# Performance work log

Measured on AMD Instinct MI355X. Metric: run time of the kernel, lower is better.

Reference implementation:

```python
import jax, jax.numpy as jnp
import numpy as np

B, P, C = 64, 196, 768   # batch, num_patches, hidden_size
HS = 384                 # hidden_s (token-mixing hidden dim)
NG = 8                   # num_grids
GMIN, GMAX = -1.0, 1.0


def _rbf(x):
    # fast-KAN radial basis: exp(-((x - grid_i)/denom)^2), grid over [GMIN, GMAX]
    grid = jnp.linspace(GMIN, GMAX, NG).astype(x.dtype)
    denom = (GMAX - GMIN) / (NG - 1)
    return jnp.exp(-jnp.square((x[..., None] - grid) / denom))  # [..., din, NG]


def _kan_linear(x, spline_w, base_w, base_b):
    # x: [..., din]; spline_w: [dout, din*NG]; base_w: [dout, din]; base_b: [dout]
    basis = _rbf(x).reshape(*x.shape[:-1], -1)          # [..., din*NG]
    out = basis @ spline_w.T                            # spline term (no bias)
    out = out + jax.nn.silu(x) @ base_w.T + base_b      # base update term
    return out


def setup_inputs() -> dict:
    key = jax.random.key(0)
    ks = jax.random.split(key, 5)
    s = 0.1  # spline_weight_init_scale
    return {
        "x": jax.random.normal(ks[0], (B, P, C), jnp.float32),
        "fc1_spline_w": jax.random.normal(ks[1], (HS, P * NG), jnp.float32) * (s / np.sqrt(P * NG)),
        "fc1_base_w": jax.random.normal(ks[2], (HS, P), jnp.float32) / np.sqrt(P),
        "fc1_base_b": jnp.zeros((HS,), jnp.float32),
        "fc2_spline_w": jax.random.normal(ks[3], (P, HS * NG), jnp.float32) * (s / np.sqrt(HS * NG)),
        "fc2_base_w": jax.random.normal(ks[4], (P, HS), jnp.float32) / np.sqrt(HS),
        "fc2_base_b": jnp.zeros((P,), jnp.float32),
    }


def reference(x, fc1_spline_w, fc1_base_w, fc1_base_b,
              fc2_spline_w, fc2_base_w, fc2_base_b):
    skip_param = 1.0
    # token mixing: permute so KANLinear acts over the patch axis
    h = jnp.swapaxes(x, 1, 2)                                   # [B, C, P]
    h = _kan_linear(h, fc1_spline_w, fc1_base_w, fc1_base_b)    # [B, C, HS]
    # dropout p=0 -> identity; the two intermediate permutes cancel
    h = _kan_linear(h, fc2_spline_w, fc2_base_w, fc2_base_b)    # [B, C, P]
    out = jnp.swapaxes(h, 1, 2)                                 # [B, P, C]
    return out + skip_param * x
```

## Files before the change

### kernel.cpp

```cpp
#include <hip/hip_runtime.h>
#include <cstdint>

#define B_  64
#define P_  196
#define C_  768
#define HS_ 384
#define M_  49152

#define NC1 13
#define KT1 111
#define NT1 12
#define NC2 24
#define KT2 216
#define NT2 7

#define H1_ELEMS  ((size_t)M_ * HS_)
#define W1P_ELEMS ((size_t)KT1 * NT1 * 512)
#define W2P_ELEMS ((size_t)KT2 * NT2 * 512)

typedef __attribute__((ext_vector_type(8)))  short short8;
typedef __attribute__((ext_vector_type(16))) float f32x16;

#define MFMA(w, a, c) __builtin_amdgcn_mfma_f32_32x32x16_bf16((w), (a), (c), 0, 0, 0)

static __device__ __forceinline__ float bf2f(unsigned short u) {
    union { unsigned int i; float f; } v; v.i = ((unsigned int)u) << 16; return v.f;
}
static __device__ __forceinline__ unsigned short f2bf_rne(float f) {
    union { float f; unsigned int i; } v; v.f = f;
    unsigned int r = v.i + 0x7FFFu + ((v.i >> 16) & 1u);
    return (unsigned short)(r >> 16);
}
static __device__ __forceinline__ unsigned int pack2(float a, float b) {
    unsigned int ua = __float_as_uint(a) + 0x8000u;
    unsigned int ub = __float_as_uint(b) + 0x8000u;
    return __builtin_amdgcn_perm(ub, ua, 0x07060302u);
}
static __device__ __forceinline__ short8 rbf8(float s) {
    float t0 = 3.5f * s + 3.5f;
    union { short8 s8; unsigned int u[4]; } r;
#pragma unroll
    for (int q = 0; q < 4; q++) {
        float d0 = t0 - (float)(2 * q);
        float d1 = t0 - (float)(2 * q + 1);
        r.u[q] = pack2(__expf(-d0 * d0), __expf(-d1 * d1));
    }
    return r.s8;
}
static __device__ __forceinline__ unsigned int silu2(float a, float b) {
    float fa = a * __builtin_amdgcn_rcpf(1.f + __expf(-a));
    float fb = b * __builtin_amdgcn_rcpf(1.f + __expf(-b));
    return pack2(fa, fb);
}

__global__ void pack_w_kernel(const float* __restrict__ w1s,
                              const float* __restrict__ w1b,
                              const float* __restrict__ w2s,
                              const float* __restrict__ w2b,
                              unsigned short* __restrict__ w1p,
                              unsigned short* __restrict__ w2p) {
    size_t idx = (size_t)blockIdx.x * 256 + threadIdx.x;
    if (idx < W1P_ELEMS) {
        int j    = idx & 7;
        int lane = (idx >> 3) & 63;
        int lin  = idx >> 9;
        int nt   = lin % NT1;
        int tt   = lin / NT1;
        int cc   = (tt < 108) ? tt / 9 : 12;
        int kk   = (tt < 108) ? tt % 9 : (tt - 108);
        int ktl  = (cc < 12) ? kk : ((kk < 2) ? kk : 8);
        int n = nt * 32 + (lane & 31);
        int khalf = lane >> 5;
        float v = 0.f;
        if (ktl < 8) {
            int p = cc * 16 + ktl * 2 + khalf;
            if (p < P_) v = w1s[(size_t)n * 1568 + p * 8 + j];
        } else {
            int p = cc * 16 + khalf * 8 + j;
            if (p < P_) v = w1b[(size_t)n * 196 + p];
        }
        w1p[idx] = f2bf_rne(v);
    } else {
        size_t idx2 = idx - W1P_ELEMS;
        if (idx2 < W2P_ELEMS) {
            int j    = idx2 & 7;
            int lane = (idx2 >> 3) & 63;
            int lin  = idx2 >> 9;
            int nt   = lin % NT2;
            int tt   = lin / NT2;
            int cc   = tt / 9;
            int ktl  = tt % 9;
            int n = nt * 32 + (lane & 31);
            int khalf = lane >> 5;
            float v = 0.f;
            if (n < P_) {
                if (ktl < 8) {
                    int s = cc * 16 + ktl * 2 + khalf;
                    v = w2s[(size_t)n * 3072 + s * 8 + j];
                } else {
                    int s = cc * 16 + khalf * 8 + j;
                    v = w2b[(size_t)n * 384 + s];
                }
            }
            w2p[idx2] = f2bf_rne(v);
        }
    }
}

#define FB_  9216

__global__ __launch_bounds__(256, 2)
void fc1_kernel(const float* __restrict__ x,
                const unsigned short* __restrict__ w1p,
                const float* __restrict__ b1,
                unsigned short* __restrict__ h1t) {
    __shared__ __align__(16) unsigned short frag[2 * FB_];
    int blk = blockIdx.x;
    int tid = threadIdx.x;
    int b   = blk / 12;
    int c0  = (blk % 12) * 64;
    const float* xb = x + (size_t)b * (P_ * C_);

    int pr  = tid & 63;
    int sg  = tid >> 6;
    int prt = pr >> 5, pl31 = pr & 31;
    int pbase_rbf  = (prt << 9) + pl31 * 8;
    int pbase_silu = 8 * 1024 + (prt << 9) + (((sg >> 1) << 5) | pl31) * 8 + (sg & 1) * 4;

    int wave = sg, lane = tid & 63;
    int l31 = lane & 31, half = lane >> 5;
    int nt0 = wave * 3;

    f32x16 acc[2][3];
#pragma unroll
    for (int rt = 0; rt < 2; rt++)
#pragma unroll
        for (int nt = 0; nt < 3; nt++)
#pragma unroll
            for (int i = 0; i < 16; i++) acc[rt][nt][i] = 0.f;

    const short8* wp = (const short8*)w1p;
    short8 wbuf[3][3];

    auto wload = [&](int d, const short8* wt0, int kk) {
        const short8* wt = wt0 + (size_t)kk * (NT1 * 64);
        wbuf[d][0] = wt[0]; wbuf[d][1] = wt[64]; wbuf[d][2] = wt[128];
    };
    auto produce = [&](int fb, const float (&rb)[4]) {
#pragma unroll
        for (int i = 0; i < 4; i++) {
            int sl = sg * 4 + i;
            *(short8*)&frag[fb + (sl >> 1) * 1024 + ((sl & 1) << 8) + pbase_rbf] = rbf8(rb[i]);
        }
        uint2 sv;
        sv.x = silu2(rb[0], rb[1]);
        sv.y = silu2(rb[2], rb[3]);
        *(uint2*)&frag[fb + pbase_silu] = sv;
    };
    auto do_mfma = [&](short8 w0, short8 w1, short8 w2, short8 a0, short8 a1) {
        acc[0][0] = MFMA(w0, a0, acc[0][0]); acc[1][0] = MFMA(w0, a1, acc[1][0]);
        acc[0][1] = MFMA(w1, a0, acc[0][1]); acc[1][1] = MFMA(w1, a1, acc[1][1]);
        acc[0][2] = MFMA(w2, a0, acc[0][2]); acc[1][2] = MFMA(w2, a1, acc[1][2]);
    };
    auto consume = [&](int fb, const short8* wt0) {
        const unsigned short* fg = &frag[fb];
        short8 a0 = *(const short8*)&fg[lane * 8];
        short8 a1 = *(const short8*)&fg[512 + lane * 8];
#pragma unroll
        for (int kk = 0; kk < 9; kk++) {
            short8 na0, na1;
            if (kk < 8) {
                na0 = *(const short8*)&fg[(kk + 1) * 1024 + lane * 8];
                na1 = *(const short8*)&fg[(kk + 1) * 1024 + 512 + lane * 8];
            }
            short8 w0 = wbuf[kk % 3][0], w1 = wbuf[kk % 3][1], w2 = wbuf[kk % 3][2];
            if (kk < 6) wload(kk % 3, wt0, kk + 3);
            do_mfma(w0, w1, w2, a0, a1);
            if (kk < 8) { a0 = na0; a1 = na1; }
        }
    };
    auto body = [&](int cc, const float (&rbP)[4], float (&rbL)[4]) {
#pragma unroll
        for (int i = 0; i < 4; i++) {
            int p = (cc + 2) * 16 + sg * 4 + i;
            p = (p < P_) ? p : (P_ - 1);
            rbL[i] = xb[(size_t)p * C_ + c0 + pr];
        }
        const short8* wt0 = wp + ((size_t)(cc * 9) * NT1 + nt0) * 64 + lane;
        wload(0, wt0, 0); wload(1, wt0, 1); wload(2, wt0, 2);
        produce(((cc + 1) & 1) * FB_, rbP);
        consume((cc & 1) * FB_, wt0);
        __syncthreads();
    };

    float rbA[4], rbB[4];
#pragma unroll
    for (int i = 0; i < 4; i++) {
        rbA[i] = xb[(size_t)(sg * 4 + i) * C_ + c0 + pr];
        rbB[i] = xb[(size_t)(16 + sg * 4 + i) * C_ + c0 + pr];
    }
    produce(0, rbA);
    __syncthreads();

    for (int c2 = 0; c2 < 6; c2++) {
        body(2 * c2,     rbB, rbA);
        body(2 * c2 + 1, rbA, rbB);
    }
    {
        const short8* wt0 = wp + ((size_t)108 * NT1 + nt0) * 64 + lane;
        wload(0, wt0, 0); wload(1, wt0, 1); wload(2, wt0, 2);
        const unsigned short* fg = &frag[0];
#pragma unroll
        for (int kk = 0; kk < 3; kk++) {
            int ktl = (kk < 2) ? kk : 8;
            short8 a0 = *(const short8*)&fg[ktl * 1024 + lane * 8];
            short8 a1 = *(const short8*)&fg[ktl * 1024 + 512 + lane * 8];
            do_mfma(wbuf[kk][0], wbuf[kk][1], wbuf[kk][2], a0, a1);
        }
    }

#pragma unroll
    for (int nt = 0; nt < 3; nt++) {
        int n0 = (nt0 + nt) * 32 + 4 * half;
#pragma unroll
        for (int reg = 0; reg < 16; reg++) {
            int n = n0 + (reg & 3) + 8 * (reg >> 2);
            float bv = b1[n];
#pragma unroll
            for (int rt = 0; rt < 2; rt++) {
                h1t[(size_t)n * M_ + blk * 64 + rt * 32 + l31] = f2bf_rne(acc[rt][nt][reg] + bv);
            }
        }
    }
}

__global__ __launch_bounds__(256, 2)
void fc2_kernel(const unsigned short* __restrict__ h1t,
                const unsigned short* __restrict__ w2p,
                const float* __restrict__ b2,
                const float* __restrict__ x,
                float* __restrict__ out) {
    __shared__ __align__(16) unsigned short frag[2 * FB_];
    int blk = blockIdx.x;
    int tid = threadIdx.x;
    int rbase = blk * 64;

    int pr  = tid & 63;
    int sg  = tid >> 6;
    int prt = pr >> 5, pl31 = pr & 31;
    int pbase_rbf  = (prt << 9) + pl31 * 8;
    int pbase_silu = 8 * 1024 + (prt << 9) + (((sg >> 1) << 5) | pl31) * 8 + (sg & 1) * 4;

    int wave = sg, lane = tid & 63;
    int l31 = lane & 31, half = lane >> 5;
    int nt0 = wave * 2;
    int ntn = (wave < 3) ? 2 : 1;
    int off1 = (ntn > 1) ? 64 : 0;

    f32x16 acc[2][2];
#pragma unroll
    for (int rt = 0; rt < 2; rt++)
#pragma unroll
        for (int nt = 0; nt < 2; nt++)
#pragma unroll
            for (int i = 0; i < 16; i++) acc[rt][nt][i] = 0.f;

    const short8* wp = (const short8*)w2p;
    short8 wbuf[3][2];

    auto wload = [&](int d, const short8* wt0, int kk) {
        const short8* wt = wt0 + (size_t)kk * (NT2 * 64);
        wbuf[d][0] = wt[0]; wbuf[d][1] = wt[off1];
    };
    auto produce = [&](int fb, const unsigned short (&rb)[4]) {
        float v0 = bf2f(rb[0]), v1 = bf2f(rb[1]), v2 = bf2f(rb[2]), v3 = bf2f(rb[3]);
        float vv[4] = {v0, v1, v2, v3};
#pragma unroll
        for (int i = 0; i < 4; i++) {
            int sl = sg * 4 + i;
            *(short8*)&frag[fb + (sl >> 1) * 1024 + ((sl & 1) << 8) + pbase_rbf] = rbf8(vv[i]);
        }
        uint2 sv;
        sv.x = silu2(v0, v1);
        sv.y = silu2(v2, v3);
        *(uint2*)&frag[fb + pbase_silu] = sv;
    };
    auto do_mfma = [&](short8 w0, short8 w1, short8 a0, short8 a1) {
        acc[0][0] = MFMA(w0, a0, acc[0][0]); acc[1][0] = MFMA(w0, a1, acc[1][0]);
        acc[0][1] = MFMA(w1, a0, acc[0][1]); acc[1][1] = MFMA(w1, a1, acc[1][1]);
    };
    auto consume = [&](int fb, const short8* wt0) {
        const unsigned short* fg = &frag[fb];
        short8 a0 = *(const short8*)&fg[lane * 8];
        short8 a1 = *(const short8*)&fg[512 + lane * 8];
#pragma unroll
        for (int kk = 0; kk < 9; kk++) {
            short8 na0, na1;
            if (kk < 8) {
                na0 = *(const short8*)&fg[(kk + 1) * 1024 + lane * 8];
                na1 = *(const short8*)&fg[(kk + 1) * 1024 + 512 + lane * 8];
            }
            short8 w0 = wbuf[kk % 3][0], w1 = wbuf[kk % 3][1];
            if (kk < 6) wload(kk % 3, wt0, kk + 3);
            do_mfma(w0, w1, a0, a1);
            if (kk < 8) { a0 = na0; a1 = na1; }
        }
    };
    auto body = [&](int cc, const unsigned short (&rbP)[4], unsigned short (&rbL)[4]) {
#pragma unroll
        for (int i = 0; i < 4; i++) {
            int s = (cc + 2) * 16 + sg * 4 + i;
            s = (s < HS_) ? s : (HS_ - 1);
            rbL[i] = h1t[(size_t)s * M_ + rbase + pr];
        }
        const short8* wt0 = wp + ((size_t)(cc * 9) * NT2 + nt0) * 64 + lane;
        wload(0, wt0, 0); wload(1, wt0, 1); wload(2, wt0, 2);
        if (cc + 1 < NC2) produce(((cc + 1) & 1) * FB_, rbP);
        consume((cc & 1) * FB_, wt0);
        __syncthreads();
    };

    unsigned short rbA[4], rbB[4];
#pragma unroll
    for (int i = 0; i < 4; i++) {
        rbA[i] = h1t[(size_t)(sg * 4 + i) * M_ + rbase + pr];
        rbB[i] = h1t[(size_t)(16 + sg * 4 + i) * M_ + rbase + pr];
    }
    produce(0, rbA);
    __syncthreads();

    for (int c2 = 0; c2 < 12; c2++) {
        body(2 * c2,     rbB, rbA);
        body(2 * c2 + 1, rbA, rbB);
    }

    int b = blk / 12;
    int c0 = (blk % 12) * 64;
#pragma unroll
    for (int nt = 0; nt < 2; nt++) {
        if (nt < ntn) {
            int p0 = (nt0 + nt) * 32 + 4 * half;
#pragma unroll
            for (int reg = 0; reg < 16; reg++) {
                int p = p0 + (reg & 3) + 8 * (reg >> 2);
                if (p < P_) {
                    float bv = b2[p];
#pragma unroll
                    for (int rt = 0; rt < 2; rt++) {
                        size_t off = ((size_t)b * P_ + p) * C_ + c0 + rt * 32 + l31;
                        out[off] = acc[rt][nt][reg] + bv + x[off];
                    }
                }
            }
        }
    }
}

extern "C" void kernel_launch(void* const* d_in, const int* in_sizes, int n_in,
                              void* d_out, int out_size, void* d_ws, size_t ws_size,
                              hipStream_t stream) {
    const float* x   = (const float*)d_in[0];
    const float* w1s = (const float*)d_in[1];
    const float* w1b = (const float*)d_in[2];
    const float* b1  = (const float*)d_in[3];
    const float* w2s = (const float*)d_in[4];
    const float* w2b = (const float*)d_in[5];
    const float* b2  = (const float*)d_in[6];
    float* out = (float*)d_out;

    unsigned short* h1t = (unsigned short*)d_ws;
    unsigned short* w1p = h1t + H1_ELEMS;
    unsigned short* w2p = w1p + W1P_ELEMS;

    int pack_blocks = (int)((W1P_ELEMS + W2P_ELEMS) / 256);
    pack_w_kernel<<<pack_blocks, 256, 0, stream>>>(w1s, w1b, w2s, w2b, w1p, w2p);
    fc1_kernel<<<M_ / 64, 256, 0, stream>>>(x, w1p, b1, h1t);
    fc2_kernel<<<M_ / 64, 256, 0, stream>>>(h1t, w2p, b2, x, out);
}
```

Baseline: 300.7 us.

## Double waves per block, splitting row tiles across waves in fc1 and fc2

```diff
diff --git a/kernel.cpp b/kernel.cpp
--- a/kernel.cpp
+++ b/kernel.cpp
@@ -109,7 +109,8 @@
 
 #define FB_  9216
 
-__global__ __launch_bounds__(256, 2)
+
+__global__ __launch_bounds__(512, 4)
 void fc1_kernel(const float* __restrict__ x,
                 const unsigned short* __restrict__ w1p,
                 const float* __restrict__ b1,
@@ -125,19 +126,19 @@
     int sg  = tid >> 6;
     int prt = pr >> 5, pl31 = pr & 31;
     int pbase_rbf  = (prt << 9) + pl31 * 8;
-    int pbase_silu = 8 * 1024 + (prt << 9) + (((sg >> 1) << 5) | pl31) * 8 + (sg & 1) * 4;
-
-    int wave = sg, lane = tid & 63;
+    int pbase_silu = 8 * 1024 + (prt << 9) + (((sg >> 2) << 5) | pl31) * 8 + (sg & 3) * 2;
+
+    int lane = tid & 63;
     int l31 = lane & 31, half = lane >> 5;
-    int nt0 = wave * 3;
-
-    f32x16 acc[2][3];
-#pragma unroll
-    for (int rt = 0; rt < 2; rt++)
-#pragma unroll
-        for (int nt = 0; nt < 3; nt++)
-#pragma unroll
-            for (int i = 0; i < 16; i++) acc[rt][nt][i] = 0.f;
+    int rt  = sg >> 2;
+    int nt0 = (sg & 3) * 3;
+    int abase = rt * 512 + lane * 8;
+
+    f32x16 acc[3];
+#pragma unroll
+    for (int nt = 0; nt < 3; nt++)
+#pragma unroll
+        for (int i = 0; i < 16; i++) acc[nt][i] = 0.f;
 
     const short8* wp = (const short8*)w1p;
     short8 wbuf[3][3];
@@ -146,43 +147,36 @@
         const short8* wt = wt0 + (size_t)kk * (NT1 * 64);
         wbuf[d][0] = wt[0]; wbuf[d][1] = wt[64]; wbuf[d][2] = wt[128];
     };
-    auto produce = [&](int fb, const float (&rb)[4]) {
-#pragma unroll
-        for (int i = 0; i < 4; i++) {
-            int sl = sg * 4 + i;
+    auto produce = [&](int fb, const float (&rb)[2]) {
+#pragma unroll
+        for (int i = 0; i < 2; i++) {
+            int sl = sg * 2 + i;
             *(short8*)&frag[fb + (sl >> 1) * 1024 + ((sl & 1) << 8) + pbase_rbf] = rbf8(rb[i]);
         }
-        uint2 sv;
-        sv.x = silu2(rb[0], rb[1]);
-        sv.y = silu2(rb[2], rb[3]);
-        *(uint2*)&frag[fb + pbase_silu] = sv;
-    };
-    auto do_mfma = [&](short8 w0, short8 w1, short8 w2, short8 a0, short8 a1) {
-        acc[0][0] = MFMA(w0, a0, acc[0][0]); acc[1][0] = MFMA(w0, a1, acc[1][0]);
-        acc[0][1] = MFMA(w1, a0, acc[0][1]); acc[1][1] = MFMA(w1, a1, acc[1][1]);
-        acc[0][2] = MFMA(w2, a0, acc[0][2]); acc[1][2] = MFMA(w2, a1, acc[1][2]);
+        *(unsigned int*)&frag[fb + pbase_silu] = silu2(rb[0], rb[1]);
+    };
+    auto do_mfma = [&](short8 w0, short8 w1, short8 w2, short8 a0) {
+        acc[0] = MFMA(w0, a0, acc[0]);
+        acc[1] = MFMA(w1, a0, acc[1]);
+        acc[2] = MFMA(w2, a0, acc[2]);
     };
     auto consume = [&](int fb, const short8* wt0) {
         const unsigned short* fg = &frag[fb];
-        short8 a0 = *(const short8*)&fg[lane * 8];
-        short8 a1 = *(const short8*)&fg[512 + lane * 8];
+        short8 a0 = *(const short8*)&fg[abase];
 #pragma unroll
         for (int kk = 0; kk < 9; kk++) {
-            short8 na0, na1;
-            if (kk < 8) {
-                na0 = *(const short8*)&fg[(kk + 1) * 1024 + lane * 8];
-                na1 = *(const short8*)&fg[(kk + 1) * 1024 + 512 + lane * 8];
-            }
+            short8 na0;
+            if (kk < 8) na0 = *(const short8*)&fg[(kk + 1) * 1024 + abase];
             short8 w0 = wbuf[kk % 3][0], w1 = wbuf[kk % 3][1], w2 = wbuf[kk % 3][2];
             if (kk < 6) wload(kk % 3, wt0, kk + 3);
-            do_mfma(w0, w1, w2, a0, a1);
-            if (kk < 8) { a0 = na0; a1 = na1; }
-        }
-    };
-    auto body = [&](int cc, const float (&rbP)[4], float (&rbL)[4]) {
-#pragma unroll
-        for (int i = 0; i < 4; i++) {
-            int p = (cc + 2) * 16 + sg * 4 + i;
+            do_mfma(w0, w1, w2, a0);
+            if (kk < 8) a0 = na0;
+        }
+    };
+    auto body = [&](int cc, const float (&rbP)[2], float (&rbL)[2]) {
+#pragma unroll
+        for (int i = 0; i < 2; i++) {
+            int p = (cc + 2) * 16 + sg * 2 + i;
             p = (p < P_) ? p : (P_ - 1);
             rbL[i] = xb[(size_t)p * C_ + c0 + pr];
         }
@@ -193,11 +187,11 @@
         __syncthreads();
     };
 
-    float rbA[4], rbB[4];
-#pragma unroll
-    for (int i = 0; i < 4; i++) {
-        rbA[i] = xb[(size_t)(sg * 4 + i) * C_ + c0 + pr];
-        rbB[i] = xb[(size_t)(16 + sg * 4 + i) * C_ + c0 + pr];
+    float rbA[2], rbB[2];
+#pragma unroll
+    for (int i = 0; i < 2; i++) {
+        rbA[i] = xb[(size_t)(sg * 2 + i) * C_ + c0 + pr];
+        rbB[i] = xb[(size_t)(16 + sg * 2 + i) * C_ + c0 + pr];
     }
     produce(0, rbA);
     __syncthreads();
@@ -213,9 +207,8 @@
 #pragma unroll
         for (int kk = 0; kk < 3; kk++) {
             int ktl = (kk < 2) ? kk : 8;
-            short8 a0 = *(const short8*)&fg[ktl * 1024 + lane * 8];
-            short8 a1 = *(const short8*)&fg[ktl * 1024 + 512 + lane * 8];
-            do_mfma(wbuf[kk][0], wbuf[kk][1], wbuf[kk][2], a0, a1);
+            short8 a0 = *(const short8*)&fg[ktl * 1024 + abase];
+            do_mfma(wbuf[kk][0], wbuf[kk][1], wbuf[kk][2], a0);
         }
     }
 
@@ -226,15 +219,12 @@
         for (int reg = 0; reg < 16; reg++) {
             int n = n0 + (reg & 3) + 8 * (reg >> 2);
             float bv = b1[n];
-#pragma unroll
-            for (int rt = 0; rt < 2; rt++) {
-                h1t[(size_t)n * M_ + blk * 64 + rt * 32 + l31] = f2bf_rne(acc[rt][nt][reg] + bv);
-            }
-        }
-    }
-}
-
-__global__ __launch_bounds__(256, 2)
+            h1t[(size_t)n * M_ + blk * 64 + rt * 32 + l31] = f2bf_rne(acc[nt][reg] + bv);
+        }
+    }
+}
+
+__global__ __launch_bounds__(512, 4)
 void fc2_kernel(const unsigned short* __restrict__ h1t,
                 const unsigned short* __restrict__ w2p,
                 const float* __restrict__ b2,
@@ -249,21 +239,22 @@
     int sg  = tid >> 6;
     int prt = pr >> 5, pl31 = pr & 31;
     int pbase_rbf  = (prt << 9) + pl31 * 8;
-    int pbase_silu = 8 * 1024 + (prt << 9) + (((sg >> 1) << 5) | pl31) * 8 + (sg & 1) * 4;
-
-    int wave = sg, lane = tid & 63;
+    int pbase_silu = 8 * 1024 + (prt << 9) + (((sg >> 2) << 5) | pl31) * 8 + (sg & 3) * 2;
+
+    int lane = tid & 63;
     int l31 = lane & 31, half = lane >> 5;
-    int nt0 = wave * 2;
-    int ntn = (wave < 3) ? 2 : 1;
-    int off1 = (ntn > 1) ? 64 : 0;
-
-    f32x16 acc[2][2];
-#pragma unroll
-    for (int rt = 0; rt < 2; rt++)
-#pragma unroll
-        for (int nt = 0; nt < 2; nt++)
-#pragma unroll
-            for (int i = 0; i < 16; i++) acc[rt][nt][i] = 0.f;
+    int rt  = sg >> 2;
+    int ntg = sg & 3;
+    int nt0 = ntg * 2;
+    bool two = (ntg < 3);
+    int off1 = two ? 64 : 0;
+    int abase = rt * 512 + lane * 8;
+
+    f32x16 acc[2];
+#pragma unroll
+    for (int nt = 0; nt < 2; nt++)
+#pragma unroll
+        for (int i = 0; i < 16; i++) acc[nt][i] = 0.f;
 
     const short8* wp = (const short8*)w2p;
     short8 wbuf[3][2];
@@ -272,44 +263,37 @@
         const short8* wt = wt0 + (size_t)kk * (NT2 * 64);
         wbuf[d][0] = wt[0]; wbuf[d][1] = wt[off1];
     };
-    auto produce = [&](int fb, const unsigned short (&rb)[4]) {
-        float v0 = bf2f(rb[0]), v1 = bf2f(rb[1]), v2 = bf2f(rb[2]), v3 = bf2f(rb[3]);
-        float vv[4] = {v0, v1, v2, v3};
-#pragma unroll
-        for (int i = 0; i < 4; i++) {
-            int sl = sg * 4 + i;
+    auto produce = [&](int fb, const unsigned short (&rb)[2]) {
+        float v0 = bf2f(rb[0]), v1 = bf2f(rb[1]);
+        float vv[2] = {v0, v1};
+#pragma unroll
+        for (int i = 0; i < 2; i++) {
+            int sl = sg * 2 + i;
             *(short8*)&frag[fb + (sl >> 1) * 1024 + ((sl & 1) << 8) + pbase_rbf] = rbf8(vv[i]);
         }
-        uint2 sv;
-        sv.x = silu2(v0, v1);
-        sv.y = silu2(v2, v3);
-        *(uint2*)&frag[fb + pbase_silu] = sv;
-    };
-    auto do_mfma = [&](short8 w0, short8 w1, short8 a0, short8 a1) {
-        acc[0][0] = MFMA(w0, a0, acc[0][0]); acc[1][0] = MFMA(w0, a1, acc[1][0]);
-        acc[0][1] = MFMA(w1, a0, acc[0][1]); acc[1][1] = MFMA(w1, a1, acc[1][1]);
+        *(unsigned int*)&frag[fb + pbase_silu] = silu2(v0, v1);
+    };
+    auto do_mfma = [&](short8 w0, short8 w1, short8 a0) {
+        acc[0] = MFMA(w0, a0, acc[0]);
+        if (two) acc[1] = MFMA(w1, a0, acc[1]);
     };
     auto consume = [&](int fb, const short8* wt0) {
         const unsigned short* fg = &frag[fb];
-        short8 a0 = *(const short8*)&fg[lane * 8];
-        short8 a1 = *(const short8*)&fg[512 + lane * 8];
+        short8 a0 = *(const short8*)&fg[abase];
 #pragma unroll
         for (int kk = 0; kk < 9; kk++) {
-            short8 na0, na1;
-            if (kk < 8) {
-                na0 = *(const short8*)&fg[(kk + 1) * 1024 + lane * 8];
-                na1 = *(const short8*)&fg[(kk + 1) * 1024 + 512 + lane * 8];
-            }
+            short8 na0;
+            if (kk < 8) na0 = *(const short8*)&fg[(kk + 1) * 1024 + abase];
             short8 w0 = wbuf[kk % 3][0], w1 = wbuf[kk % 3][1];
             if (kk < 6) wload(kk % 3, wt0, kk + 3);
-            do_mfma(w0, w1, a0, a1);
-            if (kk < 8) { a0 = na0; a1 = na1; }
-        }
-    };
-    auto body = [&](int cc, const unsigned short (&rbP)[4], unsigned short (&rbL)[4]) {
-#pragma unroll
-        for (int i = 0; i < 4; i++) {
-            int s = (cc + 2) * 16 + sg * 4 + i;
+            do_mfma(w0, w1, a0);
+            if (kk < 8) a0 = na0;
+        }
+    };
+    auto body = [&](int cc, const unsigned short (&rbP)[2], unsigned short (&rbL)[2]) {
+#pragma unroll
+        for (int i = 0; i < 2; i++) {
+            int s = (cc + 2) * 16 + sg * 2 + i;
             s = (s < HS_) ? s : (HS_ - 1);
             rbL[i] = h1t[(size_t)s * M_ + rbase + pr];
         }
@@ -320,11 +304,11 @@
         __syncthreads();
     };
 
-    unsigned short rbA[4], rbB[4];
-#pragma unroll
-    for (int i = 0; i < 4; i++) {
-        rbA[i] = h1t[(size_t)(sg * 4 + i) * M_ + rbase + pr];
-        rbB[i] = h1t[(size_t)(16 + sg * 4 + i) * M_ + rbase + pr];
+    unsigned short rbA[2], rbB[2];
+#pragma unroll
+    for (int i = 0; i < 2; i++) {
+        rbA[i] = h1t[(size_t)(sg * 2 + i) * M_ + rbase + pr];
+        rbB[i] = h1t[(size_t)(16 + sg * 2 + i) * M_ + rbase + pr];
     }
     produce(0, rbA);
     __syncthreads();
@@ -338,18 +322,15 @@
     int c0 = (blk % 12) * 64;
 #pragma unroll
     for (int nt = 0; nt < 2; nt++) {
-        if (nt < ntn) {
+        if (nt == 0 || two) {
             int p0 = (nt0 + nt) * 32 + 4 * half;
 #pragma unroll
             for (int reg = 0; reg < 16; reg++) {
                 int p = p0 + (reg & 3) + 8 * (reg >> 2);
                 if (p < P_) {
                     float bv = b2[p];
-#pragma unroll
-                    for (int rt = 0; rt < 2; rt++) {
-                        size_t off = ((size_t)b * P_ + p) * C_ + c0 + rt * 32 + l31;
-                        out[off] = acc[rt][nt][reg] + bv + x[off];
-                    }
+                    size_t off = ((size_t)b * P_ + p) * C_ + c0 + rt * 32 + l31;
+                    out[off] = acc[nt][reg] + bv + x[off];
                 }
             }
         }
@@ -374,6 +355,6 @@
 
     int pack_blocks = (int)((W1P_ELEMS + W2P_ELEMS) / 256);
     pack_w_kernel<<<pack_blocks, 256, 0, stream>>>(w1s, w1b, w2s, w2b, w1p, w2p);
-    fc1_kernel<<<M_ / 64, 256, 0, stream>>>(x, w1p, b1, h1t);
-    fc2_kernel<<<M_ / 64, 256, 0, stream>>>(h1t, w2p, b2, x, out);
-}
+    fc1_kernel<<<M_ / 64, 512, 0, stream>>>(x, w1p, b1, h1t);
+    fc2_kernel<<<M_ / 64, 512, 0, stream>>>(h1t, w2p, b2, x, out);
+}
```

Result: slower. 320.3 us (+6.5%).

## Interleave RBF/SiLU basis production with MFMA loop and use exp2 intrinsics

Applied to the files above, without the earlier changes.

```diff
diff --git a/kernel.cpp b/kernel.cpp
--- a/kernel.cpp
+++ b/kernel.cpp
@@ -37,19 +37,23 @@
     return __builtin_amdgcn_perm(ub, ua, 0x07060302u);
 }
 static __device__ __forceinline__ short8 rbf8(float s) {
-    float t0 = 3.5f * s + 3.5f;
+    const float Rr = 1.2011224087864498f;
+    const float Aa = 4.2039284307525743f;
+    float t1 = __builtin_fmaf(Aa, s, Aa);
     union { short8 s8; unsigned int u[4]; } r;
 #pragma unroll
     for (int q = 0; q < 4; q++) {
-        float d0 = t0 - (float)(2 * q);
-        float d1 = t0 - (float)(2 * q + 1);
-        r.u[q] = pack2(__expf(-d0 * d0), __expf(-d1 * d1));
+        float u0 = t1 - (float)(2 * q) * Rr;
+        float u1 = t1 - (float)(2 * q + 1) * Rr;
+        r.u[q] = pack2(__builtin_amdgcn_exp2f(-u0 * u0),
+                       __builtin_amdgcn_exp2f(-u1 * u1));
     }
     return r.s8;
 }
 static __device__ __forceinline__ unsigned int silu2(float a, float b) {
-    float fa = a * __builtin_amdgcn_rcpf(1.f + __expf(-a));
-    float fb = b * __builtin_amdgcn_rcpf(1.f + __expf(-b));
+    const float L2E = 1.4426950408889634f;
+    float fa = a * __builtin_amdgcn_rcpf(1.f + __builtin_amdgcn_exp2f(-L2E * a));
+    float fb = b * __builtin_amdgcn_rcpf(1.f + __builtin_amdgcn_exp2f(-L2E * b));
     return pack2(fa, fb);
 }
 
@@ -109,6 +113,7 @@
 
 #define FB_  9216
 
+
 __global__ __launch_bounds__(256, 2)
 void fc1_kernel(const float* __restrict__ x,
                 const unsigned short* __restrict__ w1p,
@@ -162,8 +167,11 @@
         acc[0][1] = MFMA(w1, a0, acc[0][1]); acc[1][1] = MFMA(w1, a1, acc[1][1]);
         acc[0][2] = MFMA(w2, a0, acc[0][2]); acc[1][2] = MFMA(w2, a1, acc[1][2]);
     };
-    auto consume = [&](int fb, const short8* wt0) {
-        const unsigned short* fg = &frag[fb];
+    auto body = [&](int cc, const float (&rbP)[4], float (&rbL)[4]) {
+        const short8* wt0 = wp + ((size_t)(cc * 9) * NT1 + nt0) * 64 + lane;
+        wload(0, wt0, 0); wload(1, wt0, 1); wload(2, wt0, 2);
+        int fbP = ((cc + 1) & 1) * FB_;
+        const unsigned short* fg = &frag[(cc & 1) * FB_];
         short8 a0 = *(const short8*)&fg[lane * 8];
         short8 a1 = *(const short8*)&fg[512 + lane * 8];
 #pragma unroll
@@ -175,21 +183,23 @@
             }
             short8 w0 = wbuf[kk % 3][0], w1 = wbuf[kk % 3][1], w2 = wbuf[kk % 3][2];
             if (kk < 6) wload(kk % 3, wt0, kk + 3);
+            if (kk < 4) {
+                int sl = sg * 4 + kk;
+                *(short8*)&frag[fbP + (sl >> 1) * 1024 + ((sl & 1) << 8) + pbase_rbf] = rbf8(rbP[kk]);
+            } else if (kk == 4) {
+                uint2 sv;
+                sv.x = silu2(rbP[0], rbP[1]);
+                sv.y = silu2(rbP[2], rbP[3]);
+                *(uint2*)&frag[fbP + pbase_silu] = sv;
+            } else {
+                int i = kk - 5;
+                int p = (cc + 2) * 16 + sg * 4 + i;
+                p = (p < P_) ? p : (P_ - 1);
+                rbL[i] = xb[(size_t)p * C_ + c0 + pr];
+            }
             do_mfma(w0, w1, w2, a0, a1);
             if (kk < 8) { a0 = na0; a1 = na1; }
         }
-    };
-    auto body = [&](int cc, const float (&rbP)[4], float (&rbL)[4]) {
-#pragma unroll
-        for (int i = 0; i < 4; i++) {
-            int p = (cc + 2) * 16 + sg * 4 + i;
-            p = (p < P_) ? p : (P_ - 1);
-            rbL[i] = xb[(size_t)p * C_ + c0 + pr];
-        }
-        const short8* wt0 = wp + ((size_t)(cc * 9) * NT1 + nt0) * 64 + lane;
-        wload(0, wt0, 0); wload(1, wt0, 1); wload(2, wt0, 2);
-        produce(((cc + 1) & 1) * FB_, rbP);
-        consume((cc & 1) * FB_, wt0);
         __syncthreads();
     };
 
@@ -287,10 +297,16 @@
     };
     auto do_mfma = [&](short8 w0, short8 w1, short8 a0, short8 a1) {
         acc[0][0] = MFMA(w0, a0, acc[0][0]); acc[1][0] = MFMA(w0, a1, acc[1][0]);
-        acc[0][1] = MFMA(w1, a0, acc[0][1]); acc[1][1] = MFMA(w1, a1, acc[1][1]);
-    };
-    auto consume = [&](int fb, const short8* wt0) {
-        const unsigned short* fg = &frag[fb];
+        if (ntn == 2) {
+            acc[0][1] = MFMA(w1, a0, acc[0][1]); acc[1][1] = MFMA(w1, a1, acc[1][1]);
+        }
+    };
+    auto body = [&](int cc, const unsigned short (&rbP)[4], unsigned short (&rbL)[4]) {
+        bool doProd = (cc + 1 < NC2);
+        const short8* wt0 = wp + ((size_t)(cc * 9) * NT2 + nt0) * 64 + lane;
+        wload(0, wt0, 0); wload(1, wt0, 1); wload(2, wt0, 2);
+        int fbP = ((cc + 1) & 1) * FB_;
+        const unsigned short* fg = &frag[(cc & 1) * FB_];
         short8 a0 = *(const short8*)&fg[lane * 8];
         short8 a1 = *(const short8*)&fg[512 + lane * 8];
 #pragma unroll
@@ -302,21 +318,28 @@
             }
             short8 w0 = wbuf[kk % 3][0], w1 = wbuf[kk % 3][1];
             if (kk < 6) wload(kk % 3, wt0, kk + 3);
+            if (kk < 4) {
+                if (doProd) {
+                    int sl = sg * 4 + kk;
+                    *(short8*)&frag[fbP + (sl >> 1) * 1024 + ((sl & 1) << 8) + pbase_rbf] =
+                        rbf8(bf2f(rbP[kk]));
+                }
+            } else if (kk == 4) {
+                if (doProd) {
+                    uint2 sv;
+                    sv.x = silu2(bf2f(rbP[0]), bf2f(rbP[1]));
+                    sv.y = silu2(bf2f(rbP[2]), bf2f(rbP[3]));
+                    *(uint2*)&frag[fbP + pbase_silu] = sv;
+                }
+            } else {
+                int i = kk - 5;
+                int s = (cc + 2) * 16 + sg * 4 + i;
+                s = (s < HS_) ? s : (HS_ - 1);
+                rbL[i] = h1t[(size_t)s * M_ + rbase + pr];
+            }
             do_mfma(w0, w1, a0, a1);
             if (kk < 8) { a0 = na0; a1 = na1; }
         }
-    };
-    auto body = [&](int cc, const unsigned short (&rbP)[4], unsigned short (&rbL)[4]) {
-#pragma unroll
-        for (int i = 0; i < 4; i++) {
-            int s = (cc + 2) * 16 + sg * 4 + i;
-            s = (s < HS_) ? s : (HS_ - 1);
-            rbL[i] = h1t[(size_t)s * M_ + rbase + pr];
-        }
-        const short8* wt0 = wp + ((size_t)(cc * 9) * NT2 + nt0) * 64 + lane;
-        wload(0, wt0, 0); wload(1, wt0, 1); wload(2, wt0, 2);
-        if (cc + 1 < NC2) produce(((cc + 1) & 1) * FB_, rbP);
-        consume((cc & 1) * FB_, wt0);
         __syncthreads();
     };
 
```

Result: faster. 278.7 us (-7.3%).
